# Kernel tuning notes

Hardware: AMD Instinct MI355X
Metric: run time of the kernel (lower is better)

The kernel has to match this reference:

```python
import jax, jax.numpy as jnp
import numpy as np

T = 2048      # time steps (X.shape[0])
D = 64        # input_dim (= future_dim)
H = 1024      # hidden_dim
OUT = 64      # output_dim
ND = 3        # num_decoders


def setup_inputs() -> dict:
    key = jax.random.key(0)
    ks = jax.random.split(key, 20)
    def p(k, shape, scale=0.03):
        return jax.random.normal(k, shape, dtype=jnp.float32) * scale
    return {
        "X": jax.random.normal(ks[0], (T, D), dtype=jnp.float32),
        # enc LSTMCell: input = fusion_dim = 2*D
        "enc_Wih": p(ks[1], (4 * H, 2 * D)), "enc_Whh": p(ks[2], (4 * H, H)),
        "enc_bih": p(ks[3], (4 * H,)), "enc_bhh": p(ks[4], (4 * H,)),
        # dec LSTMCell: input = H
        "dec_Wih": p(ks[5], (4 * H, H)), "dec_Whh": p(ks[6], (4 * H, H)),
        "dec_bih": p(ks[7], (4 * H,)), "dec_bhh": p(ks[8], (4 * H,)),
        # fc_relu heads
        "hx_W": p(ks[9], (H, H)), "hx_b": p(ks[10], (H,)),
        "cx_W": p(ks[11], (H, H)), "cx_b": p(ks[12], (H,)),
        "fus_W": p(ks[13], (H, OUT)), "fus_b": p(ks[14], (H,)),
        "fut_W": p(ks[15], (D, H)), "fut_b": p(ks[16], (D,)),
        # classifier (shared by encoder and decoder)
        "cls_W": p(ks[17], (OUT, H)), "cls_b": p(ks[18], (OUT,)),
    }


def _lstm_cell(x, h, c, Wih, Whh, bih, bhh):
    # torch.nn.LSTMCell gate order: i, f, g, o
    g = x @ Wih.T + bih + h @ Whh.T + bhh
    i, f, gg, o = jnp.split(g, 4, axis=-1)
    c_new = jax.nn.sigmoid(f) * c + jax.nn.sigmoid(i) * jnp.tanh(gg)
    h_new = jax.nn.sigmoid(o) * jnp.tanh(c_new)
    return h_new, c_new


def reference(X, enc_Wih, enc_Whh, enc_bih, enc_bhh,
              dec_Wih, dec_Whh, dec_bih, dec_bhh,
              hx_W, hx_b, cx_W, cx_b, fus_W, fus_b,
              fut_W, fut_b, cls_W, cls_b):
    relu = jax.nn.relu

    def step(carry, x_t):
        enc_hx, enc_cx, fut = carry  # [H], [H], [D]
        fusion = jnp.concatenate([x_t, fut])  # [2D]
        enc_hx, enc_cx = _lstm_cell(fusion, enc_hx, enc_cx,
                                    enc_Wih, enc_Whh, enc_bih, enc_bhh)
        enc_score = enc_hx @ cls_W.T + cls_b  # [OUT]
        dhx = relu(enc_hx @ hx_W.T + hx_b)
        dcx = relu(enc_cx @ cx_W.T + cx_b)
        fusion_in = jnp.zeros((H,), X.dtype)
        fut_new = jnp.zeros((D,), X.dtype)
        dscores = []
        for _ in range(ND):
            # Original bug preserved: decoder returns the UNCHANGED cx
            # (`decc_cx` typo), so dcx is never updated inside this loop.
            dhx, _unused_cx = _lstm_cell(fusion_in, dhx, dcx,
                                         dec_Wih, dec_Whh, dec_bih, dec_bhh)
            ds = dhx @ cls_W.T + cls_b
            dscores.append(ds)
            fusion_in = relu(ds @ fus_W.T + fus_b)
            fut_new = fut_new + relu(dhx @ fut_W.T + fut_b)
        fut_new = fut_new / ND
        return (enc_hx, enc_cx, fut_new), (enc_score, jnp.stack(dscores))

    init = (jnp.zeros((H,), X.dtype), jnp.zeros((H,), X.dtype),
            jnp.zeros((D,), X.dtype))
    _, (enc_scores, dec_scores) = jax.lax.scan(step, init, X[: T - ND])
    # enc_scores: [T-ND, OUT]; dec_scores: [T-ND, ND, OUT] -> [(T-ND)*ND, OUT]
    return enc_scores, dec_scores.reshape(-1, OUT)
```

## Files before the change

### kernel.cpp

```cpp
#include <hip/hip_runtime.h>
#include <hip/hip_bf16.h>


typedef unsigned short u16t;
typedef unsigned int u32t;
typedef unsigned long long u64t;

#define TSTEPS 2045
#define NWG 256
#define NTHR 512
#define SPINCAP 8192

#define HENC  0
#define CENC  4096
#define DHX   8192
#define DD1   12288
#define DD2   16384
#define SFF   20480
#define PARTF 22016

struct Params {
  const void *X, *eWih, *eWhh, *ebih, *ebhh, *dWih, *dWhh, *dbih, *dbhh,
             *hxW, *hxb, *cxW, *cxb, *fusW, *fusb_g, *futW, *futb_g, *clsW, *clsb_g;
  float* ws;
  void* out;
};

struct SharedMem {
  alignas(16) float encW[16 * 1152];
  alignas(16) u16t  decW[16 * 2048];
  alignas(16) float xs[2048];
  alignas(16) float xsf[128];
  float cls_sl[256], fut_sl[256];
  float clsb[64], futb[64], fut_acc[64], dsbuf[64], fv3[64], xnext[64];
  float bias_e[16], bias_d[16], g16[16];
  float h4[4], dcx_s[4], encc[4], hxb4[4], cxb4[4];
  int bail;
  int badcnt;
};

__device__ __forceinline__ float bfu(u16t u){
  union { u32t i; float f; } v; v.i = ((u32t)u) << 16; return v.f;
}
__device__ __forceinline__ u32t fbits(float f){
  union { float f; u32t u; } c; c.f = f; return c.u;
}
__device__ __forceinline__ u16t bf16bits(float v){
  __hip_bfloat16 b = __float2bfloat16(v);
  union { __hip_bfloat16 b; u16t u; } c; c.b = b; return c.u;
}
template<bool F32>
__device__ __forceinline__ float ldE(const void* p, int i){
  if (F32) return ((const float*)p)[i];
  return bfu(((const u16t*)p)[i]);
}
template<bool F32>
__device__ __forceinline__ u16t ldB(const void* p, int i){
  if (F32) return bf16bits(((const float*)p)[i]);
  return ((const u16t*)p)[i];
}
template<bool F32>
__device__ __forceinline__ void stO(void* p, int i, float v){
  if (F32) ((float*)p)[i] = v;
  else     ((u16t*)p)[i] = bf16bits(v);
}
__device__ __forceinline__ float sigm(float x){ return 1.f / (1.f + __expf(-x)); }
__device__ __forceinline__ float tanhx(float x){
  float e = __expf(-2.f * fabsf(x));
  float t = (1.f - e) / (1.f + e);
  return copysignf(t, x);
}
__device__ __forceinline__ void stp(float* rowbase, int idx, float v, u32t ep){
  u64t u = (u64t)fbits(v) | ((u64t)ep << 32);
  __hip_atomic_store((u64t*)rowbase + idx, u,
                     __ATOMIC_RELAXED, __HIP_MEMORY_SCOPE_AGENT);
}
__device__ __forceinline__ float4 ld4c(const float* p){
  float4 r;
  asm volatile("global_load_dwordx4 %0, %1, off sc0 sc1\n\t"
               "s_waitcnt vmcnt(0)"
               : "=&v"(r) : "v"(p) : "memory");
  return r;
}
__device__ __forceinline__ void ld4c2(const float* p0, const float* p1,
                                      float4& a, float4& b){
  asm volatile(
    "global_load_dwordx4 %0, %2, off sc0 sc1\n\t"
    "global_load_dwordx4 %1, %3, off sc0 sc1\n\t"
    "s_waitcnt vmcnt(0)"
    : "=&v"(a), "=&v"(b)
    : "v"(p0), "v"(p1)
    : "memory");
}
__device__ __forceinline__ void ld4c4(const float* p0, const float* p1,
                                      const float* p2, const float* p3,
                                      float4& r0, float4& r1, float4& r2, float4& r3){
  asm volatile(
    "global_load_dwordx4 %0, %4, off sc0 sc1\n\t"
    "global_load_dwordx4 %1, %5, off sc0 sc1\n\t"
    "global_load_dwordx4 %2, %6, off sc0 sc1\n\t"
    "global_load_dwordx4 %3, %7, off sc0 sc1\n\t"
    "s_waitcnt vmcnt(0)"
    : "=&v"(r0), "=&v"(r1), "=&v"(r2), "=&v"(r3)
    : "v"(p0), "v"(p1), "v"(p2), "v"(p3)
    : "memory");
}
__device__ __forceinline__ float2 poll2(const float* q, u32t ep, int* bail){
  float4 r; int sp = 0;
  for (;;){
    r = ld4c(q);
    if (fbits(r.y) == ep && fbits(r.w) == ep) break;
    if (*bail) break;
    if (++sp > SPINCAP){ *bail = 1; break; }
  }
  return float2{r.x, r.z};
}

template<bool F32>
__device__ __forceinline__ float hw_dot(const void* wbase, long off,
                                        const float* __restrict__ x,
                                        int K, int lane){
  float acc = 0.f;
  if (F32){
    const float* w = (const float*)wbase + off;
    for (int c = lane * 4; c < K; c += 128){
      float4 wv = *(const float4*)(w + c);
      float4 xv = *(const float4*)(x + c);
      acc = fmaf(wv.x, xv.x, acc); acc = fmaf(wv.y, xv.y, acc);
      acc = fmaf(wv.z, xv.z, acc); acc = fmaf(wv.w, xv.w, acc);
    }
  } else {
    const u16t* w = (const u16t*)wbase + off;
    for (int c = lane * 4; c < K; c += 128){
      ushort4 wv = *(const ushort4*)(w + c);
      float4  xv = *(const float4*)(x + c);
      acc = fmaf(bfu(wv.x), xv.x, acc); acc = fmaf(bfu(wv.y), xv.y, acc);
      acc = fmaf(bfu(wv.z), xv.z, acc); acc = fmaf(bfu(wv.w), xv.w, acc);
    }
  }
  #pragma unroll
  for (int o = 16; o; o >>= 1) acc += __shfl_xor(acc, o, 64);
  return acc;
}

__device__ __forceinline__ float dotnr_f32(const float* __restrict__ w,
                                           const float* __restrict__ x,
                                           int K, int lane){
  float acc = 0.f;
  for (int c = lane * 4; c < K; c += 128){
    float4 wv = *(const float4*)(w + c);
    float4 xv = *(const float4*)(x + c);
    acc = fmaf(wv.x, xv.x, acc); acc = fmaf(wv.y, xv.y, acc);
    acc = fmaf(wv.z, xv.z, acc); acc = fmaf(wv.w, xv.w, acc);
  }
  return acc;
}
__device__ __forceinline__ float wred(float a){
  #pragma unroll
  for (int o = 16; o; o >>= 1) a += __shfl_xor(a, o, 64);
  return a;
}

__device__ __forceinline__ float lds_dot_bf16(const u16t* __restrict__ w,
                                              const float* __restrict__ x,
                                              int K, int lane){
  float acc = 0.f;
  for (int c = lane * 8; c < K; c += 256){
    uint4  wv = *(const uint4*)(w + c);
    float4 x0 = *(const float4*)(x + c);
    float4 x1 = *(const float4*)(x + c + 4);
    acc = fmaf(bfu((u16t)(wv.x & 0xffff)), x0.x, acc);
    acc = fmaf(bfu((u16t)(wv.x >> 16)),    x0.y, acc);
    acc = fmaf(bfu((u16t)(wv.y & 0xffff)), x0.z, acc);
    acc = fmaf(bfu((u16t)(wv.y >> 16)),    x0.w, acc);
    acc = fmaf(bfu((u16t)(wv.z & 0xffff)), x1.x, acc);
    acc = fmaf(bfu((u16t)(wv.z >> 16)),    x1.y, acc);
    acc = fmaf(bfu((u16t)(wv.w & 0xffff)), x1.z, acc);
    acc = fmaf(bfu((u16t)(wv.w >> 16)),    x1.w, acc);
  }
  #pragma unroll
  for (int o = 16; o; o >>= 1) acc += __shfl_xor(acc, o, 64);
  return acc;
}

template<bool F32>
__device__ __forceinline__ void reduce_phase(float* ws, int ph, int par, u32t ep,
                                             int t, SharedMem& S, void* out,
                                             int w, int hw, int lane){
  const int o = (w & 7) * 16 + hw;
  const float* row = ws + PARTF + (size_t)((par * 3 + ph) * 128 + o) * 512;
  const float* q = row + lane * 16;
  float4 r0, r1, r2, r3; int sp = 0;
  for (;;){
    ld4c4(q, q + 4, q + 8, q + 12, r0, r1, r2, r3);
    if (fbits(r0.y) == ep && fbits(r0.w) == ep && fbits(r1.y) == ep &&
        fbits(r1.w) == ep && fbits(r2.y) == ep && fbits(r2.w) == ep &&
        fbits(r3.y) == ep && fbits(r3.w) == ep) break;
    if (S.bail) break;
    if (++sp > SPINCAP){ S.bail = 1; break; }
  }
  float s = r0.x + r0.z + r1.x + r1.z + r2.x + r2.z + r3.x + r3.z;
  #pragma unroll
  for (int m = 16; m; m >>= 1) s += __shfl_xor(s, m, 64);
  if (lane == 0){
    float* sf = ws + SFF + (par * 3 + ph) * 256;
    if (o < 64){
      float v = s + S.clsb[o];
      stO<F32>(out, TSTEPS * 64 + (t * 3 + ph) * 64 + o, v);
      if (ph < 2) stp(sf, o, v, ep);
    } else {
      float v = fmaxf(s + S.futb[o - 64], 0.f);
      stp(sf, o, v, ep);
    }
  }
}

template<bool F32>
__device__ void run(const Params& p, SharedMem& S){
  const int tid  = threadIdx.x;
  const int w    = blockIdx.x;
  const int hw   = tid >> 5;
  const int lane = tid & 31;
  const long grow = (long)((hw >> 2) * 1024 + 4 * w + (hw & 3));
  float* ws = p.ws;

  {
    float* er = S.encW + hw * 1152;
    for (int c = lane; c < 128; c += 32)  er[c]       = ldE<F32>(p.eWih, (int)(grow * 128 + c));
    for (int c = lane; c < 1024; c += 32) er[128 + c] = ldE<F32>(p.eWhh, (int)(grow * 1024 + c));
    u16t* dr = S.decW + hw * 2048;
    for (int c = lane; c < 1024; c += 32){
      dr[c]        = ldB<F32>(p.dWih, (int)(grow * 1024 + c));
      dr[1024 + c] = ldB<F32>(p.dWhh, (int)(grow * 1024 + c));
    }
  }
  u32t fw[64];
  float fusb0, fusb1;
  {
    int h0 = 2 * tid, h1 = 2 * tid + 1;
    #pragma unroll
    for (int o = 0; o < 64; ++o){
      u16t lo = ldB<F32>(p.fusW, h0 * 64 + o);
      u16t hi = ldB<F32>(p.fusW, h1 * 64 + o);
      fw[o] = ((u32t)hi << 16) | lo;
    }
    fusb0 = ldE<F32>(p.fusb_g, h0);
    fusb1 = ldE<F32>(p.fusb_g, h1);
  }
  if (tid < 256){
    int o = tid >> 2, j = tid & 3;
    S.cls_sl[tid] = ldE<F32>(p.clsW, o * 1024 + 4 * w + j);
    S.fut_sl[tid] = ldE<F32>(p.futW, o * 1024 + 4 * w + j);
  }
  if (tid < 64){
    S.clsb[tid] = ldE<F32>(p.clsb_g, tid);
    S.futb[tid] = ldE<F32>(p.futb_g, tid);
    S.fut_acc[tid] = 0.f;
  }
  if (tid < 16){
    int gr = (tid >> 2) * 1024 + 4 * w + (tid & 3);
    S.bias_e[tid] = ldE<F32>(p.ebih, gr) + ldE<F32>(p.ebhh, gr);
    S.bias_d[tid] = ldE<F32>(p.dbih, gr) + ldE<F32>(p.dbhh, gr);
  }
  if (tid < 4){
    S.hxb4[tid] = ldE<F32>(p.hxb, 4 * w + tid);
    S.cxb4[tid] = ldE<F32>(p.cxb, 4 * w + tid);
    S.encc[tid] = 0.f;
  }
  float enc_pre = 0.f;
  __syncthreads();

  for (int t = 0; t < TSTEPS; ++t){
    const int  par  = t & 1;
    const int  ppar = par ^ 1;
    const u32t ep   = (u32t)(t + 1);
    const u32t epv  = (u32t)t;

    if (t > 0 && tid < 32){
      const float* base = ws + SFF + (ppar * 3 + 2) * 256;
      float2 v = poll2(base + (32 + tid) * 4, epv, &S.bail);
      S.fv3[2 * tid] = v.x; S.fv3[2 * tid + 1] = v.y;
    }
    __syncthreads();
    if (tid < 64){
      S.xsf[tid] = (t == 0) ? ldE<F32>(p.X, tid) : S.xnext[tid];
      float fv = (t > 0) ? (S.fut_acc[tid] + S.fv3[tid]) * (1.f / 3.f) : 0.f;
      S.xsf[64 + tid] = fv;
      S.fut_acc[tid] = 0.f;
    }
    __syncthreads();
    {
      float a = wred(enc_pre + dotnr_f32(S.encW + hw * 1152, S.xsf, 128, lane))
              + S.bias_e[hw];
      if (lane == 0) S.g16[hw] = a;
    }
    __syncthreads();
    if (tid < 4){
      float gi = sigm(S.g16[tid]), gf = sigm(S.g16[4 + tid]),
            gg = tanhx(S.g16[8 + tid]), go = sigm(S.g16[12 + tid]);
      float c = gf * S.encc[tid] + gi * gg;
      float h = go * tanhx(c);
      S.encc[tid] = c;
      stp(ws + HENC + par * 2048, 4 * w + tid, h, ep);
      stp(ws + CENC + par * 2048, 4 * w + tid, c, ep);
    }

    {
      const float* ph_ = ws + HENC + par * 2048 + tid * 4;
      const float* pc_ = ws + CENC + par * 2048 + tid * 4;
      float4 a, b; int sp = 0;
      for (;;){
        ld4c2(ph_, pc_, a, b);
        if (fbits(a.y) == ep && fbits(a.w) == ep &&
            fbits(b.y) == ep && fbits(b.w) == ep) break;
        if (S.bail) break;
        if (++sp > SPINCAP){ S.bail = 1; break; }
      }
      S.xs[2 * tid] = a.x;        S.xs[2 * tid + 1] = a.z;
      S.xs[1024 + 2 * tid] = b.x; S.xs[1025 + 2 * tid] = b.z;
    }
    __syncthreads();
    if (hw < 4){
      float d = fmaxf(hw_dot<F32>(p.hxW, (long)(4 * w + hw) * 1024, S.xs, 1024, lane)
                      + S.hxb4[hw], 0.f);
      if (lane == 0) stp(ws + DHX + par * 2048, 4 * w + hw, d, ep);
    } else if (hw < 8){
      int j = hw - 4;
      float d = fmaxf(hw_dot<F32>(p.cxW, (long)(4 * w + j) * 1024, S.xs + 1024, 1024, lane)
                      + S.cxb4[j], 0.f);
      if (lane == 0) S.dcx_s[j] = d;
    } else if (w >= 8 && w < 16){
      int r = (w - 8) * 8 + (hw - 8);
      float s = hw_dot<F32>(p.clsW, (long)r * 1024, S.xs, 1024, lane) + S.clsb[r];
      if (lane == 0) stO<F32>(p.out, t * 64 + r, s);
    }
    enc_pre = dotnr_f32(S.encW + hw * 1152 + 128, S.xs, 1024, lane);
    __syncthreads();

    {
      float2 v = poll2(ws + DHX + par * 2048 + tid * 4, ep, &S.bail);
      S.xs[2 * tid] = v.x; S.xs[2 * tid + 1] = v.y;
    }
    __syncthreads();
    {
      float a = lds_dot_bf16(S.decW + hw * 2048 + 1024, S.xs, 1024, lane) + S.bias_d[hw];
      if (lane == 0) S.g16[hw] = a;
    }
    __syncthreads();
    if (tid < 4){
      float gi = sigm(S.g16[tid]), gf = sigm(S.g16[4 + tid]),
            gg = tanhx(S.g16[8 + tid]), go = sigm(S.g16[12 + tid]);
      float c = gf * S.dcx_s[tid] + gi * gg;
      float h = go * tanhx(c);
      S.h4[tid] = h;
      stp(ws + DD1 + par * 2048, 4 * w + tid, h, ep);
    }
    __syncthreads();
    if (tid < 64){
      float sv = 0.f, fv = 0.f;
      #pragma unroll
      for (int j = 0; j < 4; ++j){
        sv = fmaf(S.cls_sl[tid * 4 + j], S.h4[j], sv);
        fv = fmaf(S.fut_sl[tid * 4 + j], S.h4[j], fv);
      }
      float* base = ws + PARTF + (size_t)((par * 3 + 0) * 128) * 512;
      stp(base + (size_t)tid * 512,        w, sv, ep);
      stp(base + (size_t)(64 + tid) * 512, w, fv, ep);
      S.xnext[tid] = ldE<F32>(p.X, (t + 1) * 64 + tid);
    }

    for (int di = 2; di <= 3; ++di){
      const int ph = di - 2;
      {
        const float* dbuf = ws + (di == 2 ? DD1 : DD2) + par * 2048;
        float2 v = poll2(dbuf + tid * 4, ep, &S.bail);
        S.xs[1024 + 2 * tid] = v.x; S.xs[1025 + 2 * tid] = v.y;
      }
      __syncthreads();
      float accA = lds_dot_bf16(S.decW + hw * 2048 + 1024, S.xs + 1024, 1024, lane);
      if (w >= 16 + ph * 8 && w < 24 + ph * 8)
        reduce_phase<F32>(ws, ph, par, ep, t, S, p.out, w, hw, lane);
      if (tid < 64){
        const float* sf = ws + SFF + (par * 3 + ph) * 256;
        float2 v = poll2(sf + tid * 4, ep, &S.bail);
        if (tid < 32){ S.dsbuf[2 * tid] = v.x; S.dsbuf[2 * tid + 1] = v.y; }
        else { S.fv3[2 * (tid - 32)] = v.x; S.fv3[2 * (tid - 32) + 1] = v.y; }
      }
      __syncthreads();
      if (tid < 64) S.fut_acc[tid] += S.fv3[tid];
      {
        float a0 = fusb0, a1 = fusb1;
        #pragma unroll
        for (int o = 0; o < 64; ++o){
          float d = S.dsbuf[o];
          a0 = fmaf(bfu((u16t)(fw[o] & 0xffff)), d, a0);
          a1 = fmaf(bfu((u16t)(fw[o] >> 16)),    d, a1);
        }
        S.xs[2 * tid]     = fmaxf(a0, 0.f);
        S.xs[2 * tid + 1] = fmaxf(a1, 0.f);
      }
      __syncthreads();
      float accB = lds_dot_bf16(S.decW + hw * 2048, S.xs, 1024, lane);
      {
        float a = accA + accB + S.bias_d[hw];
        if (lane == 0) S.g16[hw] = a;
      }
      __syncthreads();
      if (tid < 4){
        float gi = sigm(S.g16[tid]), gf = sigm(S.g16[4 + tid]),
              gg = tanhx(S.g16[8 + tid]), go = sigm(S.g16[12 + tid]);
        float c = gf * S.dcx_s[tid] + gi * gg;
        float h = go * tanhx(c);
        S.h4[tid] = h;
        if (di == 2) stp(ws + DD2 + par * 2048, 4 * w + tid, h, ep);
      }
      __syncthreads();
      if (tid < 64){
        float sv = 0.f, fv = 0.f;
        #pragma unroll
        for (int j = 0; j < 4; ++j){
          sv = fmaf(S.cls_sl[tid * 4 + j], S.h4[j], sv);
          fv = fmaf(S.fut_sl[tid * 4 + j], S.h4[j], fv);
        }
        float* base = ws + PARTF + (size_t)((par * 3 + di - 1) * 128) * 512;
        stp(base + (size_t)tid * 512,        w, sv, ep);
        stp(base + (size_t)(64 + tid) * 512, w, fv, ep);
      }
    }
    if (w >= 32 && w < 40)
      reduce_phase<F32>(ws, 2, par, ep, t, S, p.out, w, hw, lane);
  }
}

__global__ __launch_bounds__(NTHR, 2)
void trn_persist(Params p){
  __shared__ SharedMem S;
  if (threadIdx.x == 0){ S.bail = 0; S.badcnt = 0; }
  __syncthreads();
  if (threadIdx.x < 256){
    u16t u = ((const u16t*)p.X)[threadIdx.x];
    int e = (u >> 7) & 0xff;
    if (e == 0 || e >= 141) atomicAdd(&S.badcnt, 1);
  }
  __syncthreads();
  if (S.badcnt >= 3) run<true>(p, S);
  else               run<false>(p, S);
}

extern "C" void kernel_launch(void* const* d_in, const int* in_sizes, int n_in,
                              void* d_out, int out_size, void* d_ws, size_t ws_size,
                              hipStream_t stream){
  Params P;
  P.X      = d_in[0];
  P.eWih   = d_in[1];
  P.eWhh   = d_in[2];
  P.ebih   = d_in[3];
  P.ebhh   = d_in[4];
  P.dWih   = d_in[5];
  P.dWhh   = d_in[6];
  P.dbih   = d_in[7];
  P.dbhh   = d_in[8];
  P.hxW    = d_in[9];
  P.hxb    = d_in[10];
  P.cxW    = d_in[11];
  P.cxb    = d_in[12];
  P.fusW   = d_in[13];
  P.fusb_g = d_in[14];
  P.futW   = d_in[15];
  P.futb_g = d_in[16];
  P.clsW   = d_in[17];
  P.clsb_g = d_in[18];
  P.ws     = (float*)d_ws;
  P.out    = d_out;

  void* args[] = { &P };
  hipLaunchCooperativeKernel((void*)trn_persist, dim3(NWG), dim3(NTHR),
                             args, 0, stream);
}
```

Before: 57.37 ms.

## Compute classifier/fut heads from full decoder h instead of cross-WG partial reductions

Replaces the per-workgroup partial classifier and fut-head dot products, and the reduction over 256 partials that followed, with a direct dot over the full decoder hidden vector. Only the designated workgroups compute these, reading the cls and fut weights from global memory. A third DD3 buffer is added so the last phase can read the full hidden state. Spin loops gain s_sleep backoff to reduce polling contention. This removes one barrier and the large partial-sum traffic per phase, in exchange for redundant global weight reads and longer dot products in the producer workgroups.

```diff
diff --git a/kernel.cpp b/kernel.cpp
--- a/kernel.cpp
+++ b/kernel.cpp
@@ -16,8 +16,8 @@
 #define DHX   8192
 #define DD1   12288
 #define DD2   16384
-#define SFF   20480
-#define PARTF 22016
+#define DD3   20480
+#define SFF   24576
 
 struct Params {
   const void *X, *eWih, *eWhh, *ebih, *ebhh, *dWih, *dWhh, *dbih, *dbhh,
@@ -31,10 +31,9 @@
   alignas(16) u16t  decW[16 * 2048];
   alignas(16) float xs[2048];
   alignas(16) float xsf[128];
-  float cls_sl[256], fut_sl[256];
   float clsb[64], futb[64], fut_acc[64], dsbuf[64], fv3[64], xnext[64];
   float bias_e[16], bias_d[16], g16[16];
-  float h4[4], dcx_s[4], encc[4], hxb4[4], cxb4[4];
+  float dcx_s[4], encc[4], hxb4[4], cxb4[4];
   int bail;
   int badcnt;
 };
@@ -69,6 +68,10 @@
   float e = __expf(-2.f * fabsf(x));
   float t = (1.f - e) / (1.f + e);
   return copysignf(t, x);
+}
+__device__ __forceinline__ void backoff(int sp){
+  if (sp > 8)      __builtin_amdgcn_s_sleep(8);
+  else if (sp > 2) __builtin_amdgcn_s_sleep(2);
 }
 __device__ __forceinline__ void stp(float* rowbase, int idx, float v, u32t ep){
   u64t u = (u64t)fbits(v) | ((u64t)ep << 32);
@@ -92,19 +95,6 @@
     : "v"(p0), "v"(p1)
     : "memory");
 }
-__device__ __forceinline__ void ld4c4(const float* p0, const float* p1,
-                                      const float* p2, const float* p3,
-                                      float4& r0, float4& r1, float4& r2, float4& r3){
-  asm volatile(
-    "global_load_dwordx4 %0, %4, off sc0 sc1\n\t"
-    "global_load_dwordx4 %1, %5, off sc0 sc1\n\t"
-    "global_load_dwordx4 %2, %6, off sc0 sc1\n\t"
-    "global_load_dwordx4 %3, %7, off sc0 sc1\n\t"
-    "s_waitcnt vmcnt(0)"
-    : "=&v"(r0), "=&v"(r1), "=&v"(r2), "=&v"(r3)
-    : "v"(p0), "v"(p1), "v"(p2), "v"(p3)
-    : "memory");
-}
 __device__ __forceinline__ float2 poll2(const float* q, u32t ep, int* bail){
   float4 r; int sp = 0;
   for (;;){
@@ -112,6 +102,7 @@
     if (fbits(r.y) == ep && fbits(r.w) == ep) break;
     if (*bail) break;
     if (++sp > SPINCAP){ *bail = 1; break; }
+    backoff(sp);
   }
   return float2{r.x, r.z};
 }
@@ -184,34 +175,23 @@
 }
 
 template<bool F32>
-__device__ __forceinline__ void reduce_phase(float* ws, int ph, int par, u32t ep,
-                                             int t, SharedMem& S, void* out,
-                                             int w, int hw, int lane){
+__device__ __forceinline__ void produce_sf(const Params& p, float* ws,
+                                           SharedMem& S, int ph, int par,
+                                           u32t ep, int t, int w, int hw,
+                                           int lane){
   const int o = (w & 7) * 16 + hw;
-  const float* row = ws + PARTF + (size_t)((par * 3 + ph) * 128 + o) * 512;
-  const float* q = row + lane * 16;
-  float4 r0, r1, r2, r3; int sp = 0;
-  for (;;){
-    ld4c4(q, q + 4, q + 8, q + 12, r0, r1, r2, r3);
-    if (fbits(r0.y) == ep && fbits(r0.w) == ep && fbits(r1.y) == ep &&
-        fbits(r1.w) == ep && fbits(r2.y) == ep && fbits(r2.w) == ep &&
-        fbits(r3.y) == ep && fbits(r3.w) == ep) break;
-    if (S.bail) break;
-    if (++sp > SPINCAP){ S.bail = 1; break; }
-  }
-  float s = r0.x + r0.z + r1.x + r1.z + r2.x + r2.z + r3.x + r3.z;
-  #pragma unroll
-  for (int m = 16; m; m >>= 1) s += __shfl_xor(s, m, 64);
-  if (lane == 0){
-    float* sf = ws + SFF + (par * 3 + ph) * 256;
-    if (o < 64){
-      float v = s + S.clsb[o];
-      stO<F32>(out, TSTEPS * 64 + (t * 3 + ph) * 64 + o, v);
-      if (ph < 2) stp(sf, o, v, ep);
-    } else {
-      float v = fmaxf(s + S.futb[o - 64], 0.f);
-      stp(sf, o, v, ep);
-    }
+  float* sf = ws + SFF + (par * 3 + ph) * 256;
+  if (o < 64){
+    float s = hw_dot<F32>(p.clsW, (long)o * 1024, S.xs + 1024, 1024, lane)
+            + S.clsb[o];
+    if (lane == 0){
+      stO<F32>(p.out, TSTEPS * 64 + (t * 3 + ph) * 64 + o, s);
+      if (ph < 2) stp(sf, o, s, ep);
+    }
+  } else {
+    float s = fmaxf(hw_dot<F32>(p.futW, (long)(o - 64) * 1024, S.xs + 1024, 1024, lane)
+                    + S.futb[o - 64], 0.f);
+    if (lane == 0) stp(sf, o, s, ep);
   }
 }
 
@@ -246,11 +226,6 @@
     }
     fusb0 = ldE<F32>(p.fusb_g, h0);
     fusb1 = ldE<F32>(p.fusb_g, h1);
-  }
-  if (tid < 256){
-    int o = tid >> 2, j = tid & 3;
-    S.cls_sl[tid] = ldE<F32>(p.clsW, o * 1024 + 4 * w + j);
-    S.fut_sl[tid] = ldE<F32>(p.futW, o * 1024 + 4 * w + j);
   }
   if (tid < 64){
     S.clsb[tid] = ldE<F32>(p.clsb_g, tid);
@@ -315,6 +290,7 @@
             fbits(b.y) == ep && fbits(b.w) == ep) break;
         if (S.bail) break;
         if (++sp > SPINCAP){ S.bail = 1; break; }
+        backoff(sp);
       }
       S.xs[2 * tid] = a.x;        S.xs[2 * tid + 1] = a.z;
       S.xs[1024 + 2 * tid] = b.x; S.xs[1025 + 2 * tid] = b.z;
@@ -352,22 +328,10 @@
             gg = tanhx(S.g16[8 + tid]), go = sigm(S.g16[12 + tid]);
       float c = gf * S.dcx_s[tid] + gi * gg;
       float h = go * tanhx(c);
-      S.h4[tid] = h;
       stp(ws + DD1 + par * 2048, 4 * w + tid, h, ep);
     }
-    __syncthreads();
-    if (tid < 64){
-      float sv = 0.f, fv = 0.f;
-      #pragma unroll
-      for (int j = 0; j < 4; ++j){
-        sv = fmaf(S.cls_sl[tid * 4 + j], S.h4[j], sv);
-        fv = fmaf(S.fut_sl[tid * 4 + j], S.h4[j], fv);
-      }
-      float* base = ws + PARTF + (size_t)((par * 3 + 0) * 128) * 512;
-      stp(base + (size_t)tid * 512,        w, sv, ep);
-      stp(base + (size_t)(64 + tid) * 512, w, fv, ep);
+    if (tid < 64)
       S.xnext[tid] = ldE<F32>(p.X, (t + 1) * 64 + tid);
-    }
 
     for (int di = 2; di <= 3; ++di){
       const int ph = di - 2;
@@ -377,9 +341,9 @@
         S.xs[1024 + 2 * tid] = v.x; S.xs[1025 + 2 * tid] = v.y;
       }
       __syncthreads();
+      if (w >= 16 + ph * 8 && w < 24 + ph * 8)
+        produce_sf<F32>(p, ws, S, ph, par, ep, t, w, hw, lane);
       float accA = lds_dot_bf16(S.decW + hw * 2048 + 1024, S.xs + 1024, 1024, lane);
-      if (w >= 16 + ph * 8 && w < 24 + ph * 8)
-        reduce_phase<F32>(ws, ph, par, ep, t, S, p.out, w, hw, lane);
       if (tid < 64){
         const float* sf = ws + SFF + (par * 3 + ph) * 256;
         float2 v = poll2(sf + tid * 4, ep, &S.bail);
@@ -411,24 +375,17 @@
               gg = tanhx(S.g16[8 + tid]), go = sigm(S.g16[12 + tid]);
         float c = gf * S.dcx_s[tid] + gi * gg;
         float h = go * tanhx(c);
-        S.h4[tid] = h;
-        if (di == 2) stp(ws + DD2 + par * 2048, 4 * w + tid, h, ep);
+        stp(ws + (di == 2 ? DD2 : DD3) + par * 2048, 4 * w + tid, h, ep);
+      }
+    }
+    if (w >= 32 && w < 40){
+      {
+        float2 v = poll2(ws + DD3 + par * 2048 + tid * 4, ep, &S.bail);
+        S.xs[1024 + 2 * tid] = v.x; S.xs[1025 + 2 * tid] = v.y;
       }
       __syncthreads();
-      if (tid < 64){
-        float sv = 0.f, fv = 0.f;
-        #pragma unroll
-        for (int j = 0; j < 4; ++j){
-          sv = fmaf(S.cls_sl[tid * 4 + j], S.h4[j], sv);
-          fv = fmaf(S.fut_sl[tid * 4 + j], S.h4[j], fv);
-        }
-        float* base = ws + PARTF + (size_t)((par * 3 + di - 1) * 128) * 512;
-        stp(base + (size_t)tid * 512,        w, sv, ep);
-        stp(base + (size_t)(64 + tid) * 512, w, fv, ep);
-      }
-    }
-    if (w >= 32 && w < 40)
-      reduce_phase<F32>(ws, 2, par, ep, t, S, p.out, w, hw, lane);
+      produce_sf<F32>(p, ws, S, 2, par, ep, t, w, hw, lane);
+    }
   }
 }
 
```

New measurement: 51.04 ms. -11.0%, faster.
